# Kernel tuning notes

Measured on AMD Instinct MI355X. Metric: run time of the kernel, lower is better.

The kernel has to match this reference:

```python
import jax, jax.numpy as jnp
import numpy as np

N_QUBITS = 12
FEATURE_DIM = 512
BATCH = 8192


def setup_inputs() -> dict:
    key = jax.random.key(0)
    k1, k2, k3 = jax.random.split(key, 3)
    x = jax.random.normal(k1, (BATCH, FEATURE_DIM), dtype=jnp.float32)
    W = jax.random.normal(k2, (N_QUBITS * 3, FEATURE_DIM), dtype=jnp.float32) * 0.05
    b = jax.random.normal(k3, (N_QUBITS * 3,), dtype=jnp.float32) * 0.05
    return {"x": x, "W": W, "b": b}


def _simulate(angles):
    """Batched analytic state-vector simulation.
    angles: (B, n, 3) rotation angles (RX, RY, RZ) per qubit.
    Circuit: per-qubit RX->RY->RZ on |0>, then CNOT chain (q -> q+1),
    then <Z_q> for each qubit. Wire 0 is the most significant bit
    (PennyLane default.qubit convention).
    """
    B, n, _ = angles.shape
    half = angles * 0.5
    a, be, g = half[..., 0], half[..., 1], half[..., 2]  # (B, n) each
    # RX(a)|0> = [cos(a/2), -i sin(a/2)]
    u0 = jnp.cos(a).astype(jnp.complex64)
    u1 = (-1j) * jnp.sin(a).astype(jnp.complex64)
    # RY(b) applied: [[c,-s],[s,c]]
    cb, sb = jnp.cos(be), jnp.sin(be)
    w0 = cb * u0 - sb * u1
    w1 = sb * u0 + cb * u1
    # RZ(g): diag(e^{-i g/2}, e^{+i g/2})
    ph = jnp.exp((-1j) * g.astype(jnp.complex64))
    s0 = w0 * ph
    s1 = w1 * jnp.conj(ph)
    qvecs = jnp.stack([s0, s1], axis=-1)  # (B, n, 2) single-qubit states

    # Product state via iterative kron: (B, 2^n), qubit 0 most significant.
    state = qvecs[:, 0, :]
    for q in range(1, n):
        state = (state[:, :, None] * qvecs[:, q, None, :]).reshape(B, -1)

    # CNOT chain on adjacent wires (q control, q+1 target).
    for q in range(n - 1):
        s = state.reshape(B, 2 ** q, 2, 2, -1)  # (B, lead, ctrl, tgt, rest)
        c0 = s[:, :, 0]
        c1 = s[:, :, 1, ::-1]  # flip target amplitudes when control = 1
        state = jnp.stack([c0, c1], axis=2).reshape(B, -1)

    probs = state.real ** 2 + state.imag ** 2  # (B, 2^n), float32
    # <Z_q> = sum_i probs[i] * (1 - 2*bit_q(i)), bit of wire q is MSB-first.
    idx = np.arange(2 ** n, dtype=np.int64)
    bits = (idx[:, None] >> np.arange(n - 1, -1, -1)[None, :]) & 1
    signs = jnp.asarray(1.0 - 2.0 * bits, dtype=jnp.float32)  # (2^n, n)
    return probs @ signs  # (B, n)


def reference(x, W, b):
    angles = (x @ W.T + b).reshape(x.shape[0], N_QUBITS, 3)
    return _simulate(angles)
```

## Files before the change

### kernel.cpp

```cpp
#include <hip/hip_runtime.h>


#define NQ    12
#define NDOT  24
#define KDIM  512
#define ROWS_PER_BLOCK 16

__global__ __launch_bounds__(256) void qgate_kernel(
    const float* __restrict__ x,
    const float* __restrict__ W,
    const float* __restrict__ b,
    float* __restrict__ out)
{
    __shared__ float4 wlds[NDOT * 128];

    const int tid = threadIdx.x;
    for (int i = tid; i < NDOT * 128; i += 256) {
        const int d  = i >> 7;
        const int kk = i & 127;
        const int r  = (d >> 1) * 3 + (d & 1);
        wlds[i] = reinterpret_cast<const float4*>(W)[r * 128 + kk];
    }
    __syncthreads();

    const int l   = tid & 15;
    const int row = blockIdx.x * ROWS_PER_BLOCK + (tid >> 4);

    const float4* __restrict__ xp =
        reinterpret_cast<const float4*>(x + (size_t)row * KDIM);

    float4 xv[8];
#pragma unroll
    for (int c = 0; c < 8; ++c) xv[c] = xp[c * 16 + l];

    float2 acc[NDOT];
#pragma unroll
    for (int d = 0; d < NDOT; ++d) acc[d] = make_float2(0.f, 0.f);

#pragma unroll
    for (int c = 0; c < 8; ++c) {
#pragma unroll
        for (int d = 0; d < NDOT; ++d) {
            const float4 wv = wlds[d * 128 + c * 16 + l];
            acc[d].x = fmaf(xv[c].x, wv.x, acc[d].x);
            acc[d].y = fmaf(xv[c].y, wv.y, acc[d].y);
            acc[d].x = fmaf(xv[c].z, wv.z, acc[d].x);
            acc[d].y = fmaf(xv[c].w, wv.w, acc[d].y);
        }
    }

    float s[NDOT];
#pragma unroll
    for (int d = 0; d < NDOT; ++d) {
        float v = acc[d].x + acc[d].y;
        v += __shfl_xor(v, 1);
        v += __shfl_xor(v, 2);
        v += __shfl_xor(v, 4);
        v += __shfl_xor(v, 8);
        s[d] = v;
    }

    const int j = (l < NQ) ? l : (NQ - 1);
    const float aj = s[2 * j]     + b[3 * j];
    const float bj = s[2 * j + 1] + b[3 * j + 1];
    float p = __cosf(aj) * __cosf(bj);

#pragma unroll
    for (int st = 1; st < 16; st <<= 1) {
        const float t = __shfl_up(p, st, 16);
        if (l >= st) p *= t;
    }

    if (l < NQ) out[(size_t)row * NQ + l] = p;
}

extern "C" void kernel_launch(void* const* d_in, const int* in_sizes, int n_in,
                              void* d_out, int out_size, void* d_ws, size_t ws_size,
                              hipStream_t stream) {
    const float* x = (const float*)d_in[0];
    const float* W = (const float*)d_in[1];
    const float* b = (const float*)d_in[2];
    float* out     = (float*)d_out;

    const int batch = in_sizes[0] / KDIM;
    const int grid  = batch / ROWS_PER_BLOCK;
    qgate_kernel<<<grid, 256, 0, stream>>>(x, W, b, out);
}
```

Baseline: 77.00 us.

## Process two rows per 32-lane group and use transpose-style butterfly reduction

Each 32-lane group now computes two batch rows at once, so each weight float4 read from LDS is reused for two rows' FMAs and LDS traffic per row is halved. The final cross-lane reduction is replaced by a recursive-halving exchange: each shuffle step sends one half of the partial sums and keeps the other, so every lane ends up holding the two dot products it needs instead of doing a full butterfly per dot product. This roughly halves the shuffle count. It doubles the accumulator registers, which the launch bound of two blocks per SM is meant to keep in check, at the risk of spills or lower occupancy.

New measurement: 74.01 us. -3.9%, faster.

```diff
diff --git a/kernel.cpp b/kernel.cpp
--- a/kernel.cpp
+++ b/kernel.cpp
@@ -6,7 +6,7 @@
 #define KDIM  512
 #define ROWS_PER_BLOCK 16
 
-__global__ __launch_bounds__(256) void qgate_kernel(
+__global__ __launch_bounds__(256, 2) void qgate_kernel(
     const float* __restrict__ x,
     const float* __restrict__ W,
     const float* __restrict__ b,
@@ -23,55 +23,97 @@
     }
     __syncthreads();
 
-    const int l   = tid & 15;
-    const int row = blockIdx.x * ROWS_PER_BLOCK + (tid >> 4);
+    const int l    = tid & 31;
+    const int g    = tid >> 5;
+    const int row0 = blockIdx.x * ROWS_PER_BLOCK + g * 2;
 
-    const float4* __restrict__ xp =
-        reinterpret_cast<const float4*>(x + (size_t)row * KDIM);
+    const float4* __restrict__ xp0 =
+        reinterpret_cast<const float4*>(x + (size_t)row0 * KDIM);
+    const float4* __restrict__ xp1 =
+        reinterpret_cast<const float4*>(x + (size_t)(row0 + 1) * KDIM);
 
-    float4 xv[8];
+    float4 xv0[4], xv1[4];
 #pragma unroll
-    for (int c = 0; c < 8; ++c) xv[c] = xp[c * 16 + l];
+    for (int c = 0; c < 4; ++c) { xv0[c] = xp0[c * 32 + l]; xv1[c] = xp1[c * 32 + l]; }
 
-    float2 acc[NDOT];
+    float2 a0[NDOT], a1[NDOT];
 #pragma unroll
-    for (int d = 0; d < NDOT; ++d) acc[d] = make_float2(0.f, 0.f);
+    for (int d = 0; d < NDOT; ++d) {
+        a0[d] = make_float2(0.f, 0.f);
+        a1[d] = make_float2(0.f, 0.f);
+    }
 
 #pragma unroll
-    for (int c = 0; c < 8; ++c) {
+    for (int c = 0; c < 4; ++c) {
 #pragma unroll
         for (int d = 0; d < NDOT; ++d) {
-            const float4 wv = wlds[d * 128 + c * 16 + l];
-            acc[d].x = fmaf(xv[c].x, wv.x, acc[d].x);
-            acc[d].y = fmaf(xv[c].y, wv.y, acc[d].y);
-            acc[d].x = fmaf(xv[c].z, wv.z, acc[d].x);
-            acc[d].y = fmaf(xv[c].w, wv.w, acc[d].y);
+            const float4 wv = wlds[d * 128 + c * 32 + l];
+            a0[d].x = fmaf(xv0[c].x, wv.x, a0[d].x);
+            a0[d].y = fmaf(xv0[c].y, wv.y, a0[d].y);
+            a0[d].x = fmaf(xv0[c].z, wv.z, a0[d].x);
+            a0[d].y = fmaf(xv0[c].w, wv.w, a0[d].y);
+            a1[d].x = fmaf(xv1[c].x, wv.x, a1[d].x);
+            a1[d].y = fmaf(xv1[c].y, wv.y, a1[d].y);
+            a1[d].x = fmaf(xv1[c].z, wv.z, a1[d].x);
+            a1[d].y = fmaf(xv1[c].w, wv.w, a1[d].y);
         }
     }
 
-    float s[NDOT];
+    const bool hi = (l & 16) != 0;
+    float v[32];
 #pragma unroll
     for (int d = 0; d < NDOT; ++d) {
-        float v = acc[d].x + acc[d].y;
-        v += __shfl_xor(v, 1);
-        v += __shfl_xor(v, 2);
-        v += __shfl_xor(v, 4);
-        v += __shfl_xor(v, 8);
-        s[d] = v;
+        const float s0d = a0[d].x + a0[d].y;
+        const float s1d = a1[d].x + a1[d].y;
+        const float mine  = hi ? s1d : s0d;
+        const float send  = hi ? s0d : s1d;
+        v[d] = mine + __shfl_xor(send, 16);
+    }
+#pragma unroll
+    for (int d = NDOT; d < 32; ++d) v[d] = 0.f;
+
+    float u16[16];
+#pragma unroll
+    for (int i = 0; i < 16; ++i) {
+        const float keep = (l & 8) ? v[16 + i] : v[i];
+        const float send = (l & 8) ? v[i] : v[16 + i];
+        u16[i] = keep + __shfl_xor(send, 8);
+    }
+    float u8[8];
+#pragma unroll
+    for (int i = 0; i < 8; ++i) {
+        const float keep = (l & 4) ? u16[8 + i] : u16[i];
+        const float send = (l & 4) ? u16[i] : u16[8 + i];
+        u8[i] = keep + __shfl_xor(send, 4);
+    }
+    float u4[4];
+#pragma unroll
+    for (int i = 0; i < 4; ++i) {
+        const float keep = (l & 2) ? u8[4 + i] : u8[i];
+        const float send = (l & 2) ? u8[i] : u8[4 + i];
+        u4[i] = keep + __shfl_xor(send, 2);
+    }
+    float u2[2];
+#pragma unroll
+    for (int i = 0; i < 2; ++i) {
+        const float keep = (l & 1) ? u4[2 + i] : u4[i];
+        const float send = (l & 1) ? u4[i] : u4[2 + i];
+        u2[i] = keep + __shfl_xor(send, 1);
     }
 
-    const int j = (l < NQ) ? l : (NQ - 1);
-    const float aj = s[2 * j]     + b[3 * j];
-    const float bj = s[2 * j + 1] + b[3 * j + 1];
+    const int j  = l & 15;
+    const int jc = (j < NQ) ? j : NQ - 1;
+    const float aj = u2[0] + b[3 * jc];
+    const float bj = u2[1] + b[3 * jc + 1];
     float p = __cosf(aj) * __cosf(bj);
 
 #pragma unroll
     for (int st = 1; st < 16; st <<= 1) {
         const float t = __shfl_up(p, st, 16);
-        if (l >= st) p *= t;
+        if (j >= st) p *= t;
     }
 
-    if (l < NQ) out[(size_t)row * NQ + l] = p;
+    if (j < NQ) out[(size_t)(row0 + (hi ? 1 : 0)) * NQ + j] = p;
 }
 
 extern "C" void kernel_launch(void* const* d_in, const int* in_sizes, int n_in,
```
